# Kernel optimization log

Hardware: AMD Instinct MI355X
Metric: run time of the kernel (lower is better)

## Reference

```python
import jax, jax.numpy as jnp
import numpy as np

B, C_IN, NF, H, W, L = 8, 64, 64, 96, 96, 13
NEG_SLOPE = 0.2


def conv2d(x, w, b, pad):
    # x: [B,C,H,W], w: [O,I,kh,kw]
    y = jax.lax.conv_general_dilated(
        x, w, window_strides=(1, 1), padding=[(pad, pad), (pad, pad)],
        dimension_numbers=("NCHW", "OIHW", "NCHW"))
    return y + b[None, :, None, None]


def leaky(x):
    return jax.nn.leaky_relu(x, NEG_SLOPE)


def bilinear_sample(img, px, py):
    # img: [B,C,H,W]; px,py: [B,H,W] pixel coords; zero padding outside.
    Bs, C, Hs, Ws = img.shape
    x0 = jnp.floor(px)
    y0 = jnp.floor(py)
    wx = px - x0
    wy = py - y0
    x0i = x0.astype(jnp.int32)
    y0i = y0.astype(jnp.int32)
    imgf = img.reshape(Bs, C, Hs * Ws)

    def gather(xi, yi):
        valid = ((xi >= 0) & (xi < Ws) & (yi >= 0) & (yi < Hs)).astype(img.dtype)
        xc = jnp.clip(xi, 0, Ws - 1)
        yc = jnp.clip(yi, 0, Hs - 1)
        idx = (yc * Ws + xc).reshape(Bs, 1, Hs * Ws)
        v = jnp.take_along_axis(imgf, idx, axis=2).reshape(Bs, C, Hs, Ws)
        return v * valid[:, None, :, :]

    return (gather(x0i, y0i) * ((1 - wx) * (1 - wy))[:, None]
            + gather(x0i + 1, y0i) * (wx * (1 - wy))[:, None]
            + gather(x0i, y0i + 1) * ((1 - wx) * wy)[:, None]
            + gather(x0i + 1, y0i + 1) * (wx * wy)[:, None])


def warp(img, flow):
    # img: [B,C,H,W]; flow: [B,2,H,W] (dx=flow[:,0], dy=flow[:,1])
    Bs, C, Hs, Ws = img.shape
    xx = jnp.arange(Ws, dtype=img.dtype)[None, None, :]  # [1,1,W]
    yy = jnp.arange(Hs, dtype=img.dtype)[None, :, None]  # [1,H,1]
    vx = xx + flow[:, 0]  # [B,H,W]
    vy = yy + flow[:, 1]
    # torch grid_sample(align_corners=False) with normalization 2*v/(dim-1)-1:
    # sample pixel = v*dim/(dim-1) - 0.5
    px = vx * (Ws / (Ws - 1)) - 0.5
    py = vy * (Hs / (Hs - 1)) - 0.5
    return bilinear_sample(img, px, py)


def setup_inputs() -> dict:
    key = jax.random.key(0)
    ks = jax.random.split(key, 13)
    s = 0.05
    return {
        "x": jax.random.normal(ks[0], (B, C_IN, H, W), jnp.float32),
        "m": jax.random.normal(ks[1], (B, NF, H, W), jnp.float32),
        "prev_h": jax.random.normal(ks[2], (B, NF, H, W), jnp.float32),
        "w_i2h": jax.random.normal(ks[3], (3 * NF, C_IN, 3, 3), jnp.float32) * s,
        "b_i2h": jnp.zeros((3 * NF,), jnp.float32),
        "w_i2f": jax.random.normal(ks[4], (32, C_IN, 5, 5), jnp.float32) * s,
        "b_i2f": jnp.zeros((32,), jnp.float32),
        "w_h2f": jax.random.normal(ks[5], (32, NF, 5, 5), jnp.float32) * s,
        "b_h2f": jnp.zeros((32,), jnp.float32),
        "w_fl": jax.random.normal(ks[6], (2 * L, 32, 5, 5), jnp.float32) * s,
        "b_fl": jnp.zeros((2 * L,), jnp.float32),
        "w_ret": jax.random.normal(ks[7], (3 * NF, NF * L, 1, 1), jnp.float32) * s,
        "b_ret": jnp.zeros((3 * NF,), jnp.float32),
    }


def reference(x, m, prev_h, w_i2h, b_i2h, w_i2f, b_i2f, w_h2f, b_h2f, w_fl, b_fl, w_ret, b_ret):
    # input-to-hidden gates
    i2h = conv2d(x, w_i2h, b_i2h, pad=1)              # [B,3NF,H,W]
    i0, i1, i2 = jnp.split(i2h, 3, axis=1)
    # flow generator
    f = leaky(conv2d(x, w_i2f, b_i2f, pad=2) + conv2d(prev_h, w_h2f, b_h2f, pad=2))
    flows = conv2d(f, w_fl, b_fl, pad=2)              # [B,2L,H,W]
    flows = flows.reshape(B, L, 2, H, W)
    # warp prev_h by -flow for each link (vectorized over L)
    warped = jax.vmap(lambda fl: warp(prev_h, -fl), in_axes=1, out_axes=1)(flows)
    warped = warped.reshape(B, L * NF, H, W)
    h2h = conv2d(warped, w_ret, b_ret, pad=0)         # [B,3NF,H,W]
    h0, h1, h2 = jnp.split(h2h, 3, axis=1)
    reset_gate = jax.nn.sigmoid(i0 + h0)
    update_gate = jax.nn.sigmoid(i1 + h1)
    new_mem = leaky(i2 + reset_gate * h2)
    next_h = update_gate * prev_h + (1.0 - update_gate) * new_mem
    return (next_h, m, next_h)
```

## Files before the change

### kernel.cpp

```cpp
#include <hip/hip_runtime.h>
#include <hip/hip_bf16.h>
#include <hip/hip_fp16.h>

typedef unsigned short u16;
typedef unsigned int u32;
typedef __attribute__((ext_vector_type(8))) _Float16 f16x8;
typedef __attribute__((ext_vector_type(4))) float f32x4;

#define NEG 0.2f

__device__ __forceinline__ float bf2f(u16 u) {
    return __uint_as_float(((u32)u) << 16);
}
__device__ __forceinline__ u16 f2b(float f) {
    u32 u = __float_as_uint(f);
    u32 r = (u + 0x7FFF + ((u >> 16) & 1)) >> 16;
    return (u16)r;
}
__device__ __forceinline__ u16 f2h(float f) {
    return __half_as_ushort(__float2half(f));
}
__device__ __forceinline__ float h2f(u16 u) {
    return __half2float(__ushort_as_half(u));
}
__device__ __forceinline__ float sigm(float x) {
    return 1.0f / (1.0f + __expf(-x));
}
__device__ __forceinline__ float ldin(const void* p, int idx, int flag) {
    if (flag) return ((const float*)p)[idx];
    return bf2f(((const u16*)p)[idx]);
}
__device__ __forceinline__ u16 ldin_h(const void* p, int idx, int flag) {
    if (flag) return f2h(((const float*)p)[idx]);
    return f2h(bf2f(((const u16*)p)[idx]));
}


#define WS_NEED 60371008u

__global__ void kdetect(const u16* __restrict__ x, u32* __restrict__ flag)
{
    __shared__ u32 mx[256];
    int t = threadIdx.x;
    u32 m = 0;
    for (int i = t; i < 8192; i += 256) {
        u32 e = ((u32)x[i] >> 7) & 0xFF;
        m = m > e ? m : e;
    }
    mx[t] = m;
    __syncthreads();
    for (int s = 128; s > 0; s >>= 1) {
        if (t < s) mx[t] = mx[t] > mx[t + s] ? mx[t] : mx[t + s];
        __syncthreads();
    }
    if (t == 0) flag[0] = (mx[0] > 0xC0) ? 1u : 0u;
}

__global__ void kprep(const void* __restrict__ w_i2h, const void* __restrict__ w_i2f,
                      const void* __restrict__ w_h2f, const void* __restrict__ w_fl,
                      const void* __restrict__ w_ret,
                      const void* __restrict__ b_i2h, const void* __restrict__ b_i2f,
                      const void* __restrict__ b_h2f, const void* __restrict__ b_fl,
                      const void* __restrict__ b_ret,
                      u16* __restrict__ wiA, u16* __restrict__ wfA,
                      u16* __restrict__ wlA, u16* __restrict__ wretA,
                      float* __restrict__ biases, const u32* __restrict__ flag)
{
    int flg = (int)flag[0];
    int i = blockIdx.x * 256 + threadIdx.x;
    if (i < 110592) {
        int j = i & 7; int lane = (i >> 3) & 63; int rest = i >> 9;
        int cib = rest & 1; int rest2 = rest >> 1;
        int tap = rest2 % 9; int mt = rest2 / 9;
        int oc = mt * 16 + (lane & 15);
        int ci = cib * 32 + ((lane >> 4) << 3) + j;
        wiA[i] = ldin_h(w_i2h, (oc * 64 + ci) * 9 + tap, flg);
    }
    if (i < 102400) {
        int j = i & 7; int lane = (i >> 3) & 63; int rest = i >> 9;
        int cib = rest & 3; int rest2 = rest >> 2;
        int tap = rest2 % 25; int mt = rest2 / 25;
        int oc = mt * 16 + (lane & 15);
        int cip = cib * 32 + ((lane >> 4) << 3) + j;
        wfA[i] = (cip < 64) ? ldin_h(w_i2f, (oc * 64 + cip) * 25 + tap, flg)
                            : ldin_h(w_h2f, (oc * 64 + cip - 64) * 25 + tap, flg);
    }
    if (i < 25600) {
        int j = i & 7; int lane = (i >> 3) & 63; int rest = i >> 9;
        int tap = rest % 25; int mt = rest / 25;
        int oc = mt * 16 + (lane & 15);
        int ci = ((lane >> 4) << 3) + j;
        wlA[i] = (oc < 26) ? ldin_h(w_fl, (oc * 32 + ci) * 25 + tap, flg) : (u16)0;
    }
    if (i < 159744) {
        int j = i & 7; int l = (i >> 3) & 63; int rest = i >> 9;
        int ks = rest % 26; int mt = rest / 26;
        int o = mt * 16 + (l & 15);
        int k = ks * 32 + ((l >> 4) << 3) + j;
        wretA[i] = ldin_h(w_ret, o * 832 + k, flg);
    }
    if (i < 474) {
        float v;
        if (i < 192)      v = ldin(b_i2h, i, flg);
        else if (i < 224) v = ldin(b_i2f, i - 192, flg);
        else if (i < 256) v = ldin(b_h2f, i - 224, flg);
        else if (i < 282) v = ldin(b_fl, i - 256, flg);
        else              v = ldin(b_ret, i - 282, flg);
        biases[i] = v;
    }
}

__global__ __launch_bounds__(256) void kxph(const void* __restrict__ x,
        const void* __restrict__ ph, u16* __restrict__ xph,
        const u32* __restrict__ flag)
{
    __shared__ __align__(16) u16 tile[64 * 104];
    int flg = (int)flag[0];
    int h = blockIdx.x, b = blockIdx.y;
    int t = threadIdx.x;
#pragma unroll 1
    for (int s = 0; s < 2; s++) {
        const void* src = s ? ph : x;
#pragma unroll 1
        for (int i = t; i < 768; i += 256) {
            int wc = i % 12, c = i / 12;
            int base = ((b * 64 + c) * 96 + h) * 96 + wc * 8;
            u16 r[8];
            if (flg) {
                const float* sp = (const float*)src + base;
                float4 f0 = *(const float4*)sp;
                float4 f1 = *(const float4*)(sp + 4);
                r[0] = f2h(f0.x); r[1] = f2h(f0.y); r[2] = f2h(f0.z); r[3] = f2h(f0.w);
                r[4] = f2h(f1.x); r[5] = f2h(f1.y); r[6] = f2h(f1.z); r[7] = f2h(f1.w);
            } else {
                const u16* sp = (const u16*)src + base;
                uint4 u = *(const uint4*)sp;
                r[0] = f2h(bf2f((u16)(u.x & 0xFFFF))); r[1] = f2h(bf2f((u16)(u.x >> 16)));
                r[2] = f2h(bf2f((u16)(u.y & 0xFFFF))); r[3] = f2h(bf2f((u16)(u.y >> 16)));
                r[4] = f2h(bf2f((u16)(u.z & 0xFFFF))); r[5] = f2h(bf2f((u16)(u.z >> 16)));
                r[6] = f2h(bf2f((u16)(u.w & 0xFFFF))); r[7] = f2h(bf2f((u16)(u.w >> 16)));
            }
            uint4 o;
            o.x = r[0] | ((u32)r[1] << 16); o.y = r[2] | ((u32)r[3] << 16);
            o.z = r[4] | ((u32)r[5] << 16); o.w = r[6] | ((u32)r[7] << 16);
            *(uint4*)&tile[c * 104 + wc * 8] = o;
        }
        __syncthreads();
#pragma unroll 1
        for (int i = t; i < 768; i += 256) {
            int cg = i & 7, w = i >> 3;
            u16 v[8];
#pragma unroll
            for (int k = 0; k < 8; k++) v[k] = tile[(cg * 8 + k) * 104 + w];
            uint4 o;
            o.x = v[0] | ((u32)v[1] << 16); o.y = v[2] | ((u32)v[3] << 16);
            o.z = v[4] | ((u32)v[5] << 16); o.w = v[6] | ((u32)v[7] << 16);
            *(uint4*)&xph[(((b * 96 + h) * 96 + w) << 7) + s * 64 + cg * 8] = o;
        }
        __syncthreads();
    }
}

__global__ __launch_bounds__(256) void k_i2h(const u16* __restrict__ xph,
        const u16* __restrict__ wiA, const float* __restrict__ biases,
        u16* __restrict__ i2hT)
{
    __shared__ __align__(16) u16 xl[3 * 98 * 72];
    int lin = blockIdx.x;
    int b = lin & 7;
    int h = lin >> 3;
    int t = threadIdx.x, lane = t & 63, wv = t >> 6;
    int n = lane & 15, quad = lane >> 4;

#pragma unroll 1
    for (int i = t; i < 2352; i += 256) {
        int co = i & 7; int pos = i >> 3; int xx = pos % 98; int yy = pos / 98;
        int gy = h + yy - 1, gx = xx - 1;
        uint4 v = make_uint4(0, 0, 0, 0);
        if (gy >= 0 && gy < 96 && gx >= 0 && gx < 96)
            v = *(const uint4*)&xph[((((b * 96 + gy) * 96 + gx)) << 7) + (co << 3)];
        *(uint4*)&xl[(yy * 98 + xx) * 72 + (co << 3)] = v;
    }
    __syncthreads();

    int mt0 = wv * 3;
    f32x4 acc[3][6] = {};
    const f16x8* A = (const f16x8*)wiA;
    f16x8 aC[3], aN[3];
#pragma unroll
    for (int mi = 0; mi < 3; mi++)
        aC[mi] = A[(((mt0 + mi) * 9 + 0) * 2 + 0) * 64 + lane];
#pragma unroll 1
    for (int it = 0; it < 18; it++) {
        int tap = it >> 1, cib = it & 1;
        if (it < 17) {
            int tn = it + 1; int tapn = tn >> 1, cibn = tn & 1;
#pragma unroll
            for (int mi = 0; mi < 3; mi++)
                aN[mi] = A[(((mt0 + mi) * 9 + tapn) * 2 + cibn) * 64 + lane];
        }
        int dy = tap / 3, dx = tap % 3;
        __builtin_amdgcn_s_setprio(1);
#pragma unroll
        for (int g = 0; g < 6; g++) {
            f16x8 bb = *(const f16x8*)&xl[(dy * 98 + g * 16 + n + dx) * 72 + cib * 32 + quad * 8];
#pragma unroll
            for (int mi = 0; mi < 3; mi++)
                acc[mi][g] = __builtin_amdgcn_mfma_f32_16x16x32_f16(aC[mi], bb, acc[mi][g], 0, 0, 0);
        }
        __builtin_amdgcn_s_setprio(0);
#pragma unroll
        for (int mi = 0; mi < 3; mi++) aC[mi] = aN[mi];
    }

#pragma unroll
    for (int mi = 0; mi < 3; mi++) {
        int ocb = (mt0 + mi) * 16 + quad * 4;
        float b0 = biases[ocb + 0], b1 = biases[ocb + 1];
        float b2 = biases[ocb + 2], b3 = biases[ocb + 3];
#pragma unroll
        for (int g = 0; g < 6; g++) {
            u16 p0 = f2h(acc[mi][g][0] + b0);
            u16 p1 = f2h(acc[mi][g][1] + b1);
            u16 p2 = f2h(acc[mi][g][2] + b2);
            u16 p3 = f2h(acc[mi][g][3] + b3);
            int base = (((b * 96 + h) * 96 + g * 16 + n)) * 192 + ocb;
            *(uint2*)&i2hT[base] =
                make_uint2(p0 | ((u32)p1 << 16), p2 | ((u32)p3 << 16));
        }
    }
}

__global__ __launch_bounds__(256) void k_flowfeat(const u16* __restrict__ xph,
        const u16* __restrict__ wfA, const float* __restrict__ biases,
        u16* __restrict__ fT)
{
    __shared__ __align__(16) u16 xl[8 * 20 * 136];
    int lin = blockIdx.x;
    int b = lin & 7;
    int r = lin >> 3;
    int x0 = (r % 6) * 16, y0 = (r / 6) * 4;
    int t = threadIdx.x, lane = t & 63, wv = t >> 6;
    int n = lane & 15, quad = lane >> 4;

    for (int i = t; i < 2560; i += 256) {
        int co = i & 15; int pos = i >> 4; int xx = pos % 20; int yy = pos / 20;
        int gy = y0 + yy - 2, gx = x0 + xx - 2;
        uint4 v = make_uint4(0, 0, 0, 0);
        if (gy >= 0 && gy < 96 && gx >= 0 && gx < 96)
            v = *(const uint4*)&xph[((((b * 96 + gy) * 96 + gx)) << 7) + (co << 3)];
        *(uint4*)&xl[(yy * 20 + xx) * 136 + (co << 3)] = v;
    }
    __syncthreads();

    f32x4 acc0 = {}, acc1 = {};
    const f16x8* A = (const f16x8*)wfA;
    f16x8 bbC[4], a0C[4], a1C[4];
    {
        int rowb = (wv * 20 + n) * 136 + quad * 8;
#pragma unroll
        for (int cib = 0; cib < 4; cib++) {
            bbC[cib] = *(const f16x8*)&xl[rowb + cib * 32];
            a0C[cib] = A[cib * 64 + lane];
            a1C[cib] = A[(100 + cib) * 64 + lane];
        }
    }
#pragma unroll 1
    for (int tap = 0; tap < 25; tap++) {
        f16x8 bbN[4], a0N[4], a1N[4];
        if (tap < 24) {
            int tn = tap + 1;
            int dy = tn / 5, dx = tn % 5;
            int rowb = ((wv + dy) * 20 + n + dx) * 136 + quad * 8;
#pragma unroll
            for (int cib = 0; cib < 4; cib++) {
                bbN[cib] = *(const f16x8*)&xl[rowb + cib * 32];
                a0N[cib] = A[(tn * 4 + cib) * 64 + lane];
                a1N[cib] = A[((25 + tn) * 4 + cib) * 64 + lane];
            }
        }
#pragma unroll
        for (int cib = 0; cib < 4; cib++) {
            acc0 = __builtin_amdgcn_mfma_f32_16x16x32_f16(a0C[cib], bbC[cib], acc0, 0, 0, 0);
            acc1 = __builtin_amdgcn_mfma_f32_16x16x32_f16(a1C[cib], bbC[cib], acc1, 0, 0, 0);
        }
#pragma unroll
        for (int cib = 0; cib < 4; cib++) {
            bbC[cib] = bbN[cib]; a0C[cib] = a0N[cib]; a1C[cib] = a1N[cib];
        }
    }

    int base = (((b * 96 + y0 + wv) * 96 + x0 + n)) * 32 + quad * 4;
    {
        u16 p[4];
#pragma unroll
        for (int r2 = 0; r2 < 4; r2++) {
            int oc = quad * 4 + r2;
            float v = acc0[r2] + biases[192 + oc] + biases[224 + oc];
            v = (v > 0.f) ? v : NEG * v;
            p[r2] = f2h(v);
        }
        *(uint2*)&fT[base] = make_uint2(p[0] | ((u32)p[1] << 16), p[2] | ((u32)p[3] << 16));
#pragma unroll
        for (int r2 = 0; r2 < 4; r2++) {
            int oc = 16 + quad * 4 + r2;
            float v = acc1[r2] + biases[192 + oc] + biases[224 + oc];
            v = (v > 0.f) ? v : NEG * v;
            p[r2] = f2h(v);
        }
        *(uint2*)&fT[base + 16] = make_uint2(p[0] | ((u32)p[1] << 16), p[2] | ((u32)p[3] << 16));
    }
}

__global__ __launch_bounds__(256) void k_flows(const u16* __restrict__ fT,
        const u16* __restrict__ wlA, const float* __restrict__ biases,
        float* __restrict__ flows)
{
    __shared__ __align__(16) u16 xl[8 * 20 * 40];
    int lin = blockIdx.x;
    int b = lin & 7;
    int r = lin >> 3;
    int x0 = (r % 6) * 16, y0 = (r / 6) * 4;
    int t = threadIdx.x, lane = t & 63, wv = t >> 6;
    int n = lane & 15, quad = lane >> 4;

    for (int i = t; i < 640; i += 256) {
        int co = i & 3; int pos = i >> 2; int xx = pos % 20; int yy = pos / 20;
        int gy = y0 + yy - 2, gx = x0 + xx - 2;
        uint4 v = make_uint4(0, 0, 0, 0);
        if (gy >= 0 && gy < 96 && gx >= 0 && gx < 96)
            v = *(const uint4*)&fT[((((b * 96 + gy) * 96 + gx)) << 5) + (co << 3)];
        *(uint4*)&xl[(yy * 20 + xx) * 40 + (co << 3)] = v;
    }
    __syncthreads();

    f32x4 acc0 = {}, acc1 = {};
    const f16x8* A = (const f16x8*)wlA;
#pragma unroll 5
    for (int tap = 0; tap < 25; tap++) {
        int dy = tap / 5, dx = tap % 5;
        f16x8 bb = *(const f16x8*)&xl[((wv + dy) * 20 + n + dx) * 40 + quad * 8];
        f16x8 a0 = A[tap * 64 + lane];
        f16x8 a1 = A[(25 + tap) * 64 + lane];
        acc0 = __builtin_amdgcn_mfma_f32_16x16x32_f16(a0, bb, acc0, 0, 0, 0);
        acc1 = __builtin_amdgcn_mfma_f32_16x16x32_f16(a1, bb, acc1, 0, 0, 0);
    }

    int pix = (y0 + wv) * 96 + x0 + n;
#pragma unroll
    for (int r2 = 0; r2 < 4; r2++) {
        int oc = quad * 4 + r2;
        flows[(b * 26 + oc) * 9216 + pix] = acc0[r2] + biases[256 + oc];
        int oc1 = 16 + quad * 4 + r2;
        if (oc1 < 26)
            flows[(b * 26 + oc1) * 9216 + pix] = acc1[r2] + biases[256 + oc1];
    }
}

__global__ __launch_bounds__(256) void k_fused(const float* __restrict__ flows,
        const u16* __restrict__ xph, const u16* __restrict__ i2hT,
        const u16* __restrict__ wretA, const float* __restrict__ biases,
        void* __restrict__ out, const u32* __restrict__ flag)
{
    __shared__ __align__(16) u16 wl[32 * 840];

    int flg = (int)flag[0];
    int lin = blockIdx.x;
    int b = lin & 7;
    int r = lin >> 3;
    int w0 = (r % 3) * 32;
    int h = r / 3;
    int t = threadIdx.x;
    int lane = t & 63, wv = t >> 6;
    const float S = 96.f / 95.f;
    int hrow = h * 96 + w0;

    {
        int p = t >> 3, sub = t & 7;
        const float* fl = &flows[b * 26 * 9216 + hrow + p];
        float dxv[13], dyv[13];
#pragma unroll
        for (int l = 0; l < 13; l++) {
            dxv[l] = fl[(2 * l) * 9216];
            dyv[l] = fl[(2 * l + 1) * 9216];
        }
        int c0 = 64 + sub * 8;
#pragma unroll
        for (int l = 0; l < 13; l++) {
            float px = ((float)(w0 + p) - dxv[l]) * S - 0.5f;
            float py = ((float)h - dyv[l]) * S - 0.5f;
            float fx = floorf(px), fy = floorf(py);
            int x0 = (int)fx, y0 = (int)fy;
            float wx = px - fx, wy = py - fy;
            bool xv0 = (x0 >= 0) & (x0 < 96);
            bool xv1 = (x0 >= -1) & (x0 < 95);
            bool yv0 = (y0 >= 0) & (y0 < 96);
            bool yv1 = (y0 >= -1) & (y0 < 95);
            f16x8 v00 = {}, v10 = {}, v01 = {}, v11 = {};
            if (yv0) {
                const u16* rr = &xph[((b * 96 + y0) * 96 + x0) * 128 + c0];
                if (xv0) v00 = *(const f16x8*)rr;
                if (xv1) v10 = *(const f16x8*)(rr + 128);
            }
            if (yv1) {
                const u16* rr = &xph[((b * 96 + y0 + 1) * 96 + x0) * 128 + c0];
                if (xv0) v01 = *(const f16x8*)rr;
                if (xv1) v11 = *(const f16x8*)(rr + 128);
            }
            float w00 = (1.f - wx) * (1.f - wy), w10 = wx * (1.f - wy);
            float w01 = (1.f - wx) * wy,         w11 = wx * wy;
            u16 res[8];
#pragma unroll
            for (int j = 0; j < 8; j++) {
                float v = w00 * (float)v00[j] + w10 * (float)v10[j]
                        + w01 * (float)v01[j] + w11 * (float)v11[j];
                res[j] = f2h(v);
            }
            uint4 o;
            o.x = res[0] | ((u32)res[1] << 16); o.y = res[2] | ((u32)res[3] << 16);
            o.z = res[4] | ((u32)res[5] << 16); o.w = res[6] | ((u32)res[7] << 16);
            *(uint4*)&wl[p * 840 + l * 64 + sub * 8] = o;
        }
    }
    __syncthreads();

    int n = lane & 15, q = lane >> 4;
    int mt0 = wv * 3;
    f32x4 acc[3][2] = {};
    f16x8 aC[3], aN[3];
    const f16x8* Ap = (const f16x8*)wretA;
#pragma unroll
    for (int mi = 0; mi < 3; mi++)
        aC[mi] = Ap[((mt0 + mi) * 26 + 0) * 64 + lane];
#pragma unroll 1
    for (int ks = 0; ks < 26; ks++) {
        if (ks < 25) {
#pragma unroll
            for (int mi = 0; mi < 3; mi++)
                aN[mi] = Ap[((mt0 + mi) * 26 + ks + 1) * 64 + lane];
        }
        f16x8 b0 = *(const f16x8*)&wl[n * 840 + ks * 32 + q * 8];
        f16x8 b1 = *(const f16x8*)&wl[(16 + n) * 840 + ks * 32 + q * 8];
        __builtin_amdgcn_s_setprio(1);
#pragma unroll
        for (int mi = 0; mi < 3; mi++) {
            acc[mi][0] = __builtin_amdgcn_mfma_f32_16x16x32_f16(aC[mi], b0, acc[mi][0], 0, 0, 0);
            acc[mi][1] = __builtin_amdgcn_mfma_f32_16x16x32_f16(aC[mi], b1, acc[mi][1], 0, 0, 0);
        }
        __builtin_amdgcn_s_setprio(0);
#pragma unroll
        for (int mi = 0; mi < 3; mi++) aC[mi] = aN[mi];
    }
    __syncthreads();

    float* hh = (float*)wl;
#pragma unroll
    for (int mi = 0; mi < 3; mi++) {
        int ob = (mt0 + mi) * 16 + q * 4;
#pragma unroll
        for (int ni = 0; ni < 2; ni++)
#pragma unroll
            for (int r2 = 0; r2 < 4; r2++) {
                int o = ob + r2;
                hh[o * 33 + ni * 16 + n] = acc[mi][ni][r2] + biases[282 + o];
            }
    }
    __syncthreads();

#pragma unroll 1
    for (int j = 0; j < 8; j++) {
        int i = t + 256 * j;
        int cc = i & 63, p = i >> 6;
        float h0v = hh[cc * 33 + p];
        float h1v = hh[(64 + cc) * 33 + p];
        float h2v = hh[(128 + cc) * 33 + p];
        int pix = (b * 96 + h) * 96 + w0 + p;
        float i0 = h2f(i2hT[pix * 192 + cc]);
        float i1 = h2f(i2hT[pix * 192 + 64 + cc]);
        float i2 = h2f(i2hT[pix * 192 + 128 + cc]);
        float pv = h2f(xph[(pix << 7) + 64 + cc]);
        float rg = sigm(i0 + h0v);
        float ug = sigm(i1 + h1v);
        float nm = i2 + rg * h2v;
        nm = (nm > 0.f) ? nm : NEG * nm;
        float nh = ug * pv + (1.f - ug) * nm;
        hh[cc * 33 + p] = nh;
    }
    __syncthreads();

#pragma unroll 1
    for (int j = 0; j < 8; j++) {
        int i = t + 256 * j;
        int p = i & 31, cc = i >> 5;
        float nh = hh[cc * 33 + p];
        int oidx = ((b * 64 + cc) * 96 + h) * 96 + w0 + p;
        if (flg) {
            float* of = (float*)out;
            of[oidx] = nh;
            of[oidx + 2 * 4718592] = nh;
        } else {
            u16* ob16 = (u16*)out;
            u16 v = f2b(nh);
            ob16[oidx] = v;
            ob16[oidx + 2 * 4718592] = v;
        }
    }
}

__global__ void kcopym(const uint4* __restrict__ m, uint4* __restrict__ out,
                       const u32* __restrict__ flag)
{
    int flg = (int)flag[0];
    int n4 = flg ? 1179648 : 589824;
    int stride = gridDim.x * 256;
    for (int i = blockIdx.x * 256 + threadIdx.x; i < n4; i += stride)
        out[n4 + i] = m[i];
}

extern "C" void kernel_launch(void* const* d_in, const int* in_sizes, int n_in,
                              void* d_out, int out_size, void* d_ws, size_t ws_size,
                              hipStream_t stream)
{
    const void* x     = d_in[0];
    const void* m     = d_in[1];
    const void* ph    = d_in[2];
    const void* w_i2h = d_in[3];
    const void* b_i2h = d_in[4];
    const void* w_i2f = d_in[5];
    const void* b_i2f = d_in[6];
    const void* w_h2f = d_in[7];
    const void* b_h2f = d_in[8];
    const void* w_fl  = d_in[9];
    const void* b_fl  = d_in[10];
    const void* w_ret = d_in[11];
    const void* b_ret = d_in[12];

    char* ws = (char*)d_ws;
    u32*    flag   = (u32*)  (ws + 0);
    u16*    wiA    = (u16*)  (ws + 64);
    u16*    wfA    = (u16*)  (ws + 221248);
    u16*    wlA    = (u16*)  (ws + 426048);
    u16*    wretA  = (u16*)  (ws + 477248);
    float*  biases = (float*)(ws + 796736);
    u16*    xph    = (u16*)  (ws + 798784);
    u16*    i2hT   = (u16*)  (ws + 19673152);
    u16*    fT     = (u16*)  (ws + 47984704);
    float*  flows  = (float*)(ws + 52703296);
    if (ws_size < WS_NEED) return;

    kdetect<<<1, 256, 0, stream>>>((const u16*)x, flag);
    kprep<<<624, 256, 0, stream>>>(w_i2h, w_i2f, w_h2f, w_fl, w_ret,
                                   b_i2h, b_i2f, b_h2f, b_fl, b_ret,
                                   wiA, wfA, wlA, wretA, biases, flag);
    kxph<<<dim3(96, 8), 256, 0, stream>>>(x, ph, xph, flag);
    k_i2h<<<dim3(768), 256, 0, stream>>>(xph, wiA, biases, i2hT);
    k_flowfeat<<<dim3(1152), 256, 0, stream>>>(xph, wfA, biases, fT);
    k_flows<<<dim3(1152), 256, 0, stream>>>(fT, wlA, biases, flows);
    k_fused<<<dim3(2304), 256, 0, stream>>>(flows, xph, i2hT, wretA, biases,
                                            d_out, flag);
    kcopym<<<2048, 256, 0, stream>>>((const uint4*)m, (uint4*)d_out, flag);
}
```

Baseline: 297.1 us.

## Pipeline warp gathers with MFMA per link using double-buffered LDS

Replaces the two-phase design (gather all 13 warped links into a large LDS tile, then run the 1x1 retrieval GEMM) with a per-link software pipeline. The next link's bilinear gathers are issued while the current link's two k-steps of MFMA run, using a small double-buffered LDS slab. The block's LDS footprint shrinks and launch_bounds now requests 4 blocks per CU, with the aim of higher occupancy and overlap of gather latency with compute. The cost is a __syncthreads per link and register pressure from holding prefetched gather vectors under a tighter register cap, which could cause spills.

```diff
diff --git a/kernel.cpp b/kernel.cpp
--- a/kernel.cpp
+++ b/kernel.cpp
@@ -357,12 +357,13 @@
     }
 }
 
-__global__ __launch_bounds__(256) void k_fused(const float* __restrict__ flows,
+__global__ __launch_bounds__(256, 4) void k_fused(const float* __restrict__ flows,
         const u16* __restrict__ xph, const u16* __restrict__ i2hT,
         const u16* __restrict__ wretA, const float* __restrict__ biases,
         void* __restrict__ out, const u32* __restrict__ flag)
 {
-    __shared__ __align__(16) u16 wl[32 * 840];
+    __shared__ __align__(16) u16 gb[2][32][72];
+    __shared__ __align__(16) float hh[192 * 33];
 
     int flg = (int)flag[0];
     int lin = blockIdx.x;
@@ -375,85 +376,88 @@
     const float S = 96.f / 95.f;
     int hrow = h * 96 + w0;
 
-    {
-        int p = t >> 3, sub = t & 7;
-        const float* fl = &flows[b * 26 * 9216 + hrow + p];
-        float dxv[13], dyv[13];
-#pragma unroll
-        for (int l = 0; l < 13; l++) {
-            dxv[l] = fl[(2 * l) * 9216];
-            dyv[l] = fl[(2 * l + 1) * 9216];
-        }
-        int c0 = 64 + sub * 8;
-#pragma unroll
-        for (int l = 0; l < 13; l++) {
-            float px = ((float)(w0 + p) - dxv[l]) * S - 0.5f;
-            float py = ((float)h - dyv[l]) * S - 0.5f;
-            float fx = floorf(px), fy = floorf(py);
-            int x0 = (int)fx, y0 = (int)fy;
-            float wx = px - fx, wy = py - fy;
-            bool xv0 = (x0 >= 0) & (x0 < 96);
-            bool xv1 = (x0 >= -1) & (x0 < 95);
-            bool yv0 = (y0 >= 0) & (y0 < 96);
-            bool yv1 = (y0 >= -1) & (y0 < 95);
-            f16x8 v00 = {}, v10 = {}, v01 = {}, v11 = {};
-            if (yv0) {
-                const u16* rr = &xph[((b * 96 + y0) * 96 + x0) * 128 + c0];
-                if (xv0) v00 = *(const f16x8*)rr;
-                if (xv1) v10 = *(const f16x8*)(rr + 128);
-            }
-            if (yv1) {
-                const u16* rr = &xph[((b * 96 + y0 + 1) * 96 + x0) * 128 + c0];
-                if (xv0) v01 = *(const f16x8*)rr;
-                if (xv1) v11 = *(const f16x8*)(rr + 128);
-            }
-            float w00 = (1.f - wx) * (1.f - wy), w10 = wx * (1.f - wy);
-            float w01 = (1.f - wx) * wy,         w11 = wx * wy;
+    int p = t >> 3, sub = t & 7;
+    const float* fl = &flows[b * 26 * 9216 + hrow + p];
+    const u16* xb = &xph[(b * 96) * 96 * 128 + 64 + sub * 8];
+
+    int n = lane & 15, q = lane >> 4;
+    int mt0 = wv * 3;
+    f32x4 acc[3][2] = {};
+    const f16x8* Ap = (const f16x8*)wretA;
+    const f16x8 zv = {};
+
+    f16x8 c00, c10, c01, c11; float cwx, cwy;
+    f16x8 n00, n10, n01, n11; float nwx, nwy;
+    float fdxc, fdyc, fdxn, fdyn;
+
+#define GISSUE(DX, DY, V00, V10, V01, V11, WX, WY)                         \
+    {                                                                      \
+        float px = ((float)(w0 + p) - (DX)) * S - 0.5f;                    \
+        float py = ((float)h - (DY)) * S - 0.5f;                           \
+        float fx = floorf(px), fy = floorf(py);                            \
+        int ix = (int)fx, iy = (int)fy;                                    \
+        WX = px - fx; WY = py - fy;                                        \
+        bool xv0 = (ix >= 0) & (ix < 96);                                  \
+        bool xv1 = (ix >= -1) & (ix < 95);                                 \
+        bool yv0 = (iy >= 0) & (iy < 96);                                  \
+        bool yv1 = (iy >= -1) & (iy < 95);                                 \
+        V00 = zv; V10 = zv; V01 = zv; V11 = zv;                            \
+        if (yv0) {                                                         \
+            const u16* rr = xb + (iy * 96 + ix) * 128;                     \
+            if (xv0) V00 = *(const f16x8*)rr;                              \
+            if (xv1) V10 = *(const f16x8*)(rr + 128);                      \
+        }                                                                  \
+        if (yv1) {                                                         \
+            const u16* rr = xb + ((iy + 1) * 96 + ix) * 128;               \
+            if (xv0) V01 = *(const f16x8*)rr;                              \
+            if (xv1) V11 = *(const f16x8*)(rr + 128);                      \
+        }                                                                  \
+    }
+
+    fdxc = fl[0 * 9216]; fdyc = fl[1 * 9216];
+    fdxn = fl[2 * 9216]; fdyn = fl[3 * 9216];
+    GISSUE(fdxc, fdyc, c00, c10, c01, c11, cwx, cwy);
+
+#pragma unroll
+    for (int l = 0; l < 13; l++) {
+        float fdx2 = 0.f, fdy2 = 0.f;
+        if (l + 2 < 13) { fdx2 = fl[(2 * l + 4) * 9216]; fdy2 = fl[(2 * l + 5) * 9216]; }
+        if (l + 1 < 13) GISSUE(fdxn, fdyn, n00, n10, n01, n11, nwx, nwy);
+        {
+            float w00 = (1.f - cwx) * (1.f - cwy), w10 = cwx * (1.f - cwy);
+            float w01 = (1.f - cwx) * cwy,         w11 = cwx * cwy;
             u16 res[8];
 #pragma unroll
             for (int j = 0; j < 8; j++) {
-                float v = w00 * (float)v00[j] + w10 * (float)v10[j]
-                        + w01 * (float)v01[j] + w11 * (float)v11[j];
+                float v = w00 * (float)c00[j] + w10 * (float)c10[j]
+                        + w01 * (float)c01[j] + w11 * (float)c11[j];
                 res[j] = f2h(v);
             }
             uint4 o;
             o.x = res[0] | ((u32)res[1] << 16); o.y = res[2] | ((u32)res[3] << 16);
             o.z = res[4] | ((u32)res[5] << 16); o.w = res[6] | ((u32)res[7] << 16);
-            *(uint4*)&wl[p * 840 + l * 64 + sub * 8] = o;
-        }
-    }
-    __syncthreads();
-
-    int n = lane & 15, q = lane >> 4;
-    int mt0 = wv * 3;
-    f32x4 acc[3][2] = {};
-    f16x8 aC[3], aN[3];
-    const f16x8* Ap = (const f16x8*)wretA;
-#pragma unroll
-    for (int mi = 0; mi < 3; mi++)
-        aC[mi] = Ap[((mt0 + mi) * 26 + 0) * 64 + lane];
-#pragma unroll 1
-    for (int ks = 0; ks < 26; ks++) {
-        if (ks < 25) {
-#pragma unroll
-            for (int mi = 0; mi < 3; mi++)
-                aN[mi] = Ap[((mt0 + mi) * 26 + ks + 1) * 64 + lane];
-        }
-        f16x8 b0 = *(const f16x8*)&wl[n * 840 + ks * 32 + q * 8];
-        f16x8 b1 = *(const f16x8*)&wl[(16 + n) * 840 + ks * 32 + q * 8];
+            *(uint4*)&gb[l & 1][p][sub * 8] = o;
+        }
+        __syncthreads();
         __builtin_amdgcn_s_setprio(1);
 #pragma unroll
-        for (int mi = 0; mi < 3; mi++) {
-            acc[mi][0] = __builtin_amdgcn_mfma_f32_16x16x32_f16(aC[mi], b0, acc[mi][0], 0, 0, 0);
-            acc[mi][1] = __builtin_amdgcn_mfma_f32_16x16x32_f16(aC[mi], b1, acc[mi][1], 0, 0, 0);
+        for (int ksl = 0; ksl < 2; ksl++) {
+            int ks = 2 * l + ksl;
+            f16x8 b0 = *(const f16x8*)&gb[l & 1][n][ksl * 32 + q * 8];
+            f16x8 b1 = *(const f16x8*)&gb[l & 1][16 + n][ksl * 32 + q * 8];
+#pragma unroll
+            for (int mi = 0; mi < 3; mi++) {
+                f16x8 a = Ap[((mt0 + mi) * 26 + ks) * 64 + lane];
+                acc[mi][0] = __builtin_amdgcn_mfma_f32_16x16x32_f16(a, b0, acc[mi][0], 0, 0, 0);
+                acc[mi][1] = __builtin_amdgcn_mfma_f32_16x16x32_f16(a, b1, acc[mi][1], 0, 0, 0);
+            }
         }
         __builtin_amdgcn_s_setprio(0);
-#pragma unroll
-        for (int mi = 0; mi < 3; mi++) aC[mi] = aN[mi];
-    }
-    __syncthreads();
-
-    float* hh = (float*)wl;
+        c00 = n00; c10 = n10; c01 = n01; c11 = n11; cwx = nwx; cwy = nwy;
+        fdxc = fdxn; fdyc = fdyn; fdxn = fdx2; fdyn = fdy2;
+    }
+#undef GISSUE
+
 #pragma unroll
     for (int mi = 0; mi < 3; mi++) {
         int ob = (mt0 + mi) * 16 + q * 4;
@@ -470,11 +474,11 @@
 #pragma unroll 1
     for (int j = 0; j < 8; j++) {
         int i = t + 256 * j;
-        int cc = i & 63, p = i >> 6;
-        float h0v = hh[cc * 33 + p];
-        float h1v = hh[(64 + cc) * 33 + p];
-        float h2v = hh[(128 + cc) * 33 + p];
-        int pix = (b * 96 + h) * 96 + w0 + p;
+        int cc = i & 63, pp = i >> 6;
+        float h0v = hh[cc * 33 + pp];
+        float h1v = hh[(64 + cc) * 33 + pp];
+        float h2v = hh[(128 + cc) * 33 + pp];
+        int pix = (b * 96 + h) * 96 + w0 + pp;
         float i0 = h2f(i2hT[pix * 192 + cc]);
         float i1 = h2f(i2hT[pix * 192 + 64 + cc]);
         float i2 = h2f(i2hT[pix * 192 + 128 + cc]);
@@ -484,16 +488,16 @@
         float nm = i2 + rg * h2v;
         nm = (nm > 0.f) ? nm : NEG * nm;
         float nh = ug * pv + (1.f - ug) * nm;
-        hh[cc * 33 + p] = nh;
+        hh[cc * 33 + pp] = nh;
     }
     __syncthreads();
 
 #pragma unroll 1
     for (int j = 0; j < 8; j++) {
         int i = t + 256 * j;
-        int p = i & 31, cc = i >> 5;
-        float nh = hh[cc * 33 + p];
-        int oidx = ((b * 64 + cc) * 96 + h) * 96 + w0 + p;
+        int pp = i & 31, cc = i >> 5;
+        float nh = hh[cc * 33 + pp];
+        int oidx = ((b * 64 + cc) * 96 + h) * 96 + w0 + pp;
         if (flg) {
             float* of = (float*)out;
             of[oidx] = nh;
```

After: 293.0 us. Within noise of the previous version (-1.4%).
